# Kernel optimization log

Measured on AMD Instinct MI355X. Metric: run time of the kernel, lower is better.

Reference implementation:

```python
import jax, jax.numpy as jnp
import numpy as np

THRESH = 1.0   # snntorch Leaky default threshold
SLOPE = 25.0   # surrogate.fast_sigmoid(slope=25)
DIM_HEAD = 64
SCALE = DIM_HEAD ** -0.5

# snn.Leaky single step from zero membrane: mem = beta*0 + input = input,
# spike = heaviside(mem - threshold); backward uses fast_sigmoid surrogate.
@jax.custom_vjp
def spike_fn(mem):
    return (mem > THRESH).astype(mem.dtype)

def _spike_fwd(mem):
    return (mem > THRESH).astype(mem.dtype), mem

def _spike_bwd(mem, g):
    return (g / (SLOPE * jnp.abs(mem - THRESH) + 1.0) ** 2,)

spike_fn.defvjp(_spike_fwd, _spike_bwd)

def layer_norm2(x, gamma, beta, eps=1e-5):
    # torch F.layer_norm over x.shape[1:] (last two dims jointly);
    # gamma.repeat(rows,1) == broadcast of gamma over the row axis.
    m = x.mean(axis=(-2, -1), keepdims=True)
    v = x.var(axis=(-2, -1), keepdims=True)
    return (x - m) / jnp.sqrt(v + eps) * gamma + beta

def interp_linear(x, out_len):
    # F.interpolate(mode='linear', align_corners=False) over last axis
    L = x.shape[-1]
    j = jnp.arange(out_len, dtype=x.dtype)
    src = jnp.maximum((j + 0.5) * (L / out_len) - 0.5, 0.0)
    i0 = jnp.clip(jnp.floor(src).astype(jnp.int32), 0, L - 1)
    i1 = jnp.clip(i0 + 1, 0, L - 1)
    w = src - i0.astype(x.dtype)
    return x[..., i0] * (1.0 - w) + x[..., i1] * w

def setup_inputs() -> dict:
    key = jax.random.key(0)
    ks = jax.random.split(key, 8)
    H, N, DIM, HEADS, DH = 4, 512, 8192, 2, 64
    inner = HEADS * DH  # 128; H*inner = 512 (matches fc/conv dims)
    return {
        "pic": jax.random.normal(ks[0], (H, N, DIM), jnp.float32),
        "context": jax.random.normal(ks[1], (H, N, DIM), jnp.float32),
        "gamma": jnp.ones((DIM,), jnp.float32),
        "ln_beta": jnp.zeros((DIM,), jnp.float32),
        "W_pic": jax.random.normal(ks[2], (inner, DIM), jnp.float32) * 0.01,
        "b_pic": jnp.zeros((inner,), jnp.float32),
        "W_ctx": jax.random.normal(ks[3], (2 * DH, DIM), jnp.float32) * 0.01,
        "b_ctx": jnp.zeros((2 * DH,), jnp.float32),
        "conv1_w": jax.random.normal(ks[4], (32, N, 1), jnp.float32) * 0.04,
        "conv1_b": jnp.zeros((32,), jnp.float32),
        "conv2_w": jax.random.normal(ks[5], (1, 32, 1), jnp.float32) * 0.17,
        "conv2_b": jnp.zeros((1,), jnp.float32),
        "fc_w": jax.random.normal(ks[6], (N, N), jnp.float32) * 0.04,
        "fc_b": jnp.zeros((N,), jnp.float32),
    }

def reference(pic, context, gamma, ln_beta, W_pic, b_pic, W_ctx, b_ctx,
              conv1_w, conv1_b, conv2_w, conv2_b, fc_w, fc_b):
    pic = layer_norm2(pic, gamma, ln_beta)          # (H,N,DIM)
    context = layer_norm2(context, gamma, ln_beta)
    # num_steps = batch_size = 1: one SNN step, stack adds leading 'b'=1 axis
    ip_spk = spike_fn(pic)[None]                    # (1,H,N,DIM)
    ic_spk = spike_fn(context)[None]
    ip = (jnp.einsum('bhnd,od->bhno', ip_spk, W_pic) + b_pic) * SCALE  # (1,H,N,128)
    ctx = jnp.einsum('bhnd,od->bhno', ic_spk, W_ctx) + b_ctx           # (1,H,N,128)
    ic, V = jnp.split(ctx, 2, axis=-1)              # (1,H,N,64) each
    # einsum 'b h i d, b h i j -> b h i d': reduce j then broadcast-multiply
    sim = ip * ic.sum(-1, keepdims=True)            # (1,H,N,128)
    attn = jax.nn.softmax(sim, axis=-1)             # (sim - amax then softmax)
    # einsum 'b h i j, b h i d -> b h i j'
    out = attn * V.sum(-1, keepdims=True)           # (1,H,N,128)
    b, h, n, d = out.shape
    out = jnp.transpose(out, (0, 2, 1, 3)).reshape(b, n, h * d)  # (1,512,512)
    ip_sum = ip.sum(axis=3)                         # (1,H,512)
    # resnet: two kernel-size-1 Conv1d == channel-mixing matmuls
    o1 = jnp.einsum('bcl,oc->bol', out, conv1_w[:, :, 0]) + conv1_b[None, :, None]
    o1 = jnp.einsum('bcl,oc->bol', o1, conv2_w[:, :, 0]) + conv2_b[None, :, None]  # (1,1,512)
    o1 = o1 @ fc_w.T + fc_b                         # (1,1,512)
    o1 = o1 + ip_sum                                # broadcast -> (1,H,512)
    o1 = jnp.transpose(o1, (0, 2, 1))               # (1,512,H)
    o1 = interp_linear(o1, 64)                      # (1,512,64)
    ic_sum = ic.sum(axis=1)                         # (1,512,64)
    return jax.nn.relu(jax.nn.relu(o1) + ic_sum)
```

## Files before the change

kernel.cpp:

```cpp
#include <hip/hip_runtime.h>

typedef unsigned short ushort;
typedef unsigned int uint;
typedef __attribute__((ext_vector_type(8))) short short8v;
typedef __attribute__((ext_vector_type(4))) float floatx4;

#define DIMK   8192
#define NPER   512
#define NROWS  2048
#define NCOLS  128
#define KSPLIT 8
#define KCHUNK 1024
#define BK     64
#define NIT    16
#define SLICE_ELEMS 4194304.0

static const size_t STATS_OFF = 0;
static const size_t WB_OFF    = 256;
static const size_t WB_BYTES  = (size_t)2 * 128 * DIMK * 2;
static const size_t P_OFF     = WB_OFF + WB_BYTES;
static const size_t P_BYTES   = (size_t)2 * KSPLIT * NROWS * NCOLS * 4;
static const size_t OUT2_OFF  = P_OFF + P_BYTES;
static const size_t IPSUM_OFF = OUT2_OFF + (size_t)512 * 512 * 4;
static const size_t CTXB_OFF  = IPSUM_OFF + (size_t)4 * 512 * 4;
static const size_t O2_OFF    = CTXB_OFF + (size_t)2048 * 64 * 4;
static const size_t WS_NEED   = O2_OFF + (size_t)512 * 4;

__device__ __forceinline__ ushort f2bf(float x) {
  uint u = __float_as_uint(x);
  return (ushort)((u + 0x7FFFu + ((u >> 16) & 1u)) >> 16);
}

__global__ __launch_bounds__(256) void k_wconv(const float* __restrict__ Wp,
                                               const float* __restrict__ Wc,
                                               ushort* __restrict__ Wb) {
  const size_t i = ((size_t)blockIdx.x * 256 + threadIdx.x) * 8;
  const size_t HALF = (size_t)128 * DIMK;
  const float* src = (i < HALF) ? (Wp + i) : (Wc + (i - HALF));
  float4 a = *(const float4*)src;
  float4 b = *(const float4*)(src + 4);
  short8v v;
  v[0] = (short)f2bf(a.x); v[1] = (short)f2bf(a.y);
  v[2] = (short)f2bf(a.z); v[3] = (short)f2bf(a.w);
  v[4] = (short)f2bf(b.x); v[5] = (short)f2bf(b.y);
  v[6] = (short)f2bf(b.z); v[7] = (short)f2bf(b.w);
  *(short8v*)&Wb[i] = v;
}

__global__ __launch_bounds__(256) void k_stats(const float* __restrict__ pic,
                                               const float* __restrict__ ctx,
                                               double* __restrict__ stats) {
  int b = blockIdx.x;
  int s = b >> 8;
  int c = b & 255;
  int t = s >> 2, h = s & 3;
  const float* base = (t ? ctx : pic) + (size_t)h * NPER * DIMK + (size_t)c * 16384;
  const float4* p4 = reinterpret_cast<const float4*>(base);
  int tid = threadIdx.x;
  float sum = 0.f, sq = 0.f;
#pragma unroll
  for (int i = 0; i < 16; ++i) {
    float4 v = p4[tid + 256 * i];
    sum += (v.x + v.y) + (v.z + v.w);
    sq  += (v.x * v.x + v.y * v.y) + (v.z * v.z + v.w * v.w);
  }
#pragma unroll
  for (int d = 1; d < 64; d <<= 1) {
    sum += __shfl_xor(sum, d);
    sq  += __shfl_xor(sq, d);
  }
  __shared__ float ps[4], pq[4];
  int w = tid >> 6;
  if ((tid & 63) == 0) { ps[w] = sum; pq[w] = sq; }
  __syncthreads();
  if (tid == 0) {
    double S = (double)ps[0] + (double)ps[1] + (double)ps[2] + (double)ps[3];
    double Q = (double)pq[0] + (double)pq[1] + (double)pq[2] + (double)pq[3];
    atomicAdd(&stats[2 * s], S);
    atomicAdd(&stats[2 * s + 1], Q);
  }
}

__global__ __launch_bounds__(256) void k_gemm(const float* __restrict__ pic,
                                              const float* __restrict__ ctxin,
                                              const float* __restrict__ gamma,
                                              const float* __restrict__ lnbeta,
                                              const ushort* __restrict__ Wb,
                                              const double* __restrict__ stats,
                                              float* __restrict__ P) {
  const int tid  = threadIdx.x;
  const int lane = tid & 63;
  const int wv   = tid >> 6;
  const int wm   = wv >> 1, wn = wv & 1;
  const int bx = blockIdx.x, ky = blockIdx.y, t = blockIdx.z;
  const float*  A  = t ? ctxin : pic;
  const ushort* Wt = Wb + (size_t)t * 128 * DIMK;
  const int row0 = bx * 128;

  const int sidx = t * 4 + (bx >> 2);
  double su = stats[2 * sidx], qu = stats[2 * sidx + 1];
  double dmean = su * (1.0 / SLICE_ELEMS);
  const float mean = (float)dmean;
  const float var  = (float)(qu * (1.0 / SLICE_ELEMS) - dmean * dmean);
  const float rstd = rsqrtf(var + 1e-5f);

  __shared__ __align__(16) ushort Asl[2][128 * BK];
  __shared__ __align__(16) ushort Wsl[2][128 * BK];

  const int k8 = tid & 7;
  const int r0 = tid >> 3;

  const int kg8 = (lane >> 4) << 3;
  int abase[4], axor[4], bbase[4], bxor[4];
#pragma unroll
  for (int m = 0; m < 4; ++m) {
    int ra = wm * 64 + m * 16 + (lane & 15);
    abase[m] = ra * BK; axor[m] = (ra & 7) << 3;
    int rb = wn * 64 + m * 16 + (lane & 15);
    bbase[m] = rb * BK; bxor[m] = (rb & 7) << 3;
  }

  floatx4 acc[4][4];
  floatx4 zz = {0.f, 0.f, 0.f, 0.f};
#pragma unroll
  for (int m = 0; m < 4; ++m)
#pragma unroll
    for (int n = 0; n < 4; ++n) acc[m][n] = zz;

  float4 xa[4][2]; uint4 xw[4];
  float4 g0, g1, bb0, bb1;

  auto LOAD = [&](int it) {
    const int kb = ky * KCHUNK + it * BK;
    const float* gp = gamma  + kb + k8 * 8;
    const float* bp = lnbeta + kb + k8 * 8;
    g0 = *(const float4*)gp;  g1 = *(const float4*)(gp + 4);
    bb0 = *(const float4*)bp; bb1 = *(const float4*)(bp + 4);
#pragma unroll
    for (int c = 0; c < 4; ++c) {
      const int r = r0 + c * 32;
      const float* ap = A + (size_t)(row0 + r) * DIMK + kb + k8 * 8;
      xa[c][0] = *(const float4*)ap;
      xa[c][1] = *(const float4*)(ap + 4);
      xw[c] = *(const uint4*)(Wt + (size_t)r * DIMK + kb + k8 * 8);
    }
  };

  auto WRITE = [&](int buf) {
#pragma unroll
    for (int c = 0; c < 4; ++c) {
      const int r = r0 + c * 32;
      float xs[8] = {xa[c][0].x, xa[c][0].y, xa[c][0].z, xa[c][0].w,
                     xa[c][1].x, xa[c][1].y, xa[c][1].z, xa[c][1].w};
      float gs[8] = {g0.x, g0.y, g0.z, g0.w, g1.x, g1.y, g1.z, g1.w};
      float bs[8] = {bb0.x, bb0.y, bb0.z, bb0.w, bb1.x, bb1.y, bb1.z, bb1.w};
      short8v sv;
#pragma unroll
      for (int j = 0; j < 8; ++j)
        sv[j] = (short)(((xs[j] - mean) * rstd * gs[j] + bs[j] > 1.0f) ? 0x3F80 : 0);
      const int off = r * BK + ((k8 * 8) ^ ((r & 7) << 3));
      *(short8v*)&Asl[buf][off] = sv;
      *(uint4*)&Wsl[buf][off]   = xw[c];
    }
  };

  auto COMPUTE = [&](int buf) {
#pragma unroll
    for (int ks = 0; ks < 2; ++ks) {
      short8v af[4], bfr[4];
#pragma unroll
      for (int m = 0; m < 4; ++m)
        af[m] = *(const short8v*)&Asl[buf][abase[m] + ((ks * 32 + kg8) ^ axor[m])];
#pragma unroll
      for (int n = 0; n < 4; ++n)
        bfr[n] = *(const short8v*)&Wsl[buf][bbase[n] + ((ks * 32 + kg8) ^ bxor[n])];
#pragma unroll
      for (int m = 0; m < 4; ++m)
#pragma unroll
        for (int n = 0; n < 4; ++n)
          acc[m][n] = __builtin_amdgcn_mfma_f32_16x16x32_bf16(af[m], bfr[n], acc[m][n], 0, 0, 0);
    }
  };

  LOAD(0);
  WRITE(0);
  __syncthreads();
#pragma unroll 2
  for (int it = 0; it < NIT - 1; ++it) {
    LOAD(it + 1);
    COMPUTE(it & 1);
    __syncthreads();
    WRITE((it + 1) & 1);
    __syncthreads();
  }
  COMPUTE((NIT - 1) & 1);

  float* Pt = P + ((size_t)(t * KSPLIT + ky) * NROWS + row0) * NCOLS;
#pragma unroll
  for (int m = 0; m < 4; ++m) {
    const int gr = wm * 64 + m * 16 + ((lane >> 4) << 2);
#pragma unroll
    for (int n = 0; n < 4; ++n) {
      const int gc = wn * 64 + n * 16 + (lane & 15);
#pragma unroll
      for (int j = 0; j < 4; ++j)
        Pt[(size_t)(gr + j) * NCOLS + gc] = acc[m][n][j];
    }
  }
}

__global__ __launch_bounds__(128) void k_row(const float* __restrict__ P,
                                             const float* __restrict__ b_pic,
                                             const float* __restrict__ b_ctx,
                                             float* __restrict__ out2,
                                             float* __restrict__ ipsum,
                                             float* __restrict__ ctxbuf) {
  const int r = blockIdx.x;
  const int o = threadIdx.x;
  float ipv = b_pic[o];
  float cv  = b_ctx[o];
#pragma unroll
  for (int ks = 0; ks < KSPLIT; ++ks) {
    ipv += P[((size_t)ks * NROWS + r) * NCOLS + o];
    cv  += P[((size_t)(KSPLIT + ks) * NROWS + r) * NCOLS + o];
  }
  ipv *= 0.125f;

  __shared__ float sh[4];
  __shared__ float sh2[2];
  const int w = o >> 6;

  float cs = cv;
  float is = ipv;
#pragma unroll
  for (int d = 1; d < 64; d <<= 1) {
    cs += __shfl_xor(cs, d);
    is += __shfl_xor(is, d);
  }
  if ((o & 63) == 0) { sh[w] = cs; sh[2 + w] = is; }
  __syncthreads();
  const float ic_s = sh[0];
  const float v_s  = sh[1];
  const float ips  = sh[2] + sh[3];
  if (o == 0) ipsum[r] = ips;

  const float sim = ipv * ic_s;
  float m = sim;
#pragma unroll
  for (int d = 1; d < 64; d <<= 1) m = fmaxf(m, __shfl_xor(m, d));
  if ((o & 63) == 0) sh2[w] = m;
  __syncthreads();
  m = fmaxf(sh2[0], sh2[1]);
  const float e = __expf(sim - m);
  float es = e;
#pragma unroll
  for (int d = 1; d < 64; d <<= 1) es += __shfl_xor(es, d);
  if ((o & 63) == 0) sh[w] = es;
  __syncthreads();
  const float denom = sh[0] + sh[1];
  const float outv = (e / denom) * v_s;

  const int hh = r >> 9, n = r & 511;
  out2[(size_t)n * 512 + hh * 128 + o] = outv;
  if (o < 64) ctxbuf[(size_t)r * 64 + o] = cv;
}

__global__ __launch_bounds__(512) void k_mid(const float* __restrict__ out2,
                                             const float* __restrict__ c1w,
                                             const float* __restrict__ c1b,
                                             const float* __restrict__ c2w,
                                             const float* __restrict__ c2b,
                                             float* __restrict__ o2buf) {
  const int b = blockIdx.x;
  const int tid = threadIdx.x;
  __shared__ float wsh[64];
  __shared__ float c2s[32];
  if (tid < 32) c2s[tid] = c2w[tid];
  __syncthreads();
  if (tid < 64) {
    const int n = b * 64 + tid;
    float a = 0.f;
#pragma unroll
    for (int o = 0; o < 32; ++o) a += c2s[o] * c1w[o * 512 + n];
    wsh[tid] = a;
  }
  __syncthreads();
  float acc = 0.f;
#pragma unroll 8
  for (int u = 0; u < 64; ++u)
    acc += out2[(size_t)(b * 64 + u) * 512 + tid] * wsh[u];
  if (b == 0) {
    float beff = c2b[0];
#pragma unroll
    for (int o = 0; o < 32; ++o) beff += c2s[o] * c1b[o];
    acc += beff;
  }
  atomicAdd(&o2buf[tid], acc);
}

__global__ __launch_bounds__(64) void k_final(const float* __restrict__ o2buf,
                                              const float* __restrict__ fcw,
                                              const float* __restrict__ fcb,
                                              const float* __restrict__ ipsum,
                                              const float* __restrict__ ctxbuf,
                                              float* __restrict__ out) {
  const int i = blockIdx.x;
  const int j = threadIdx.x;
  float a = 0.f;
#pragma unroll
  for (int u = 0; u < 8; ++u) {
    const int k = j * 8 + u;
    a += o2buf[k] * fcw[(size_t)i * 512 + k];
  }
#pragma unroll
  for (int d = 1; d < 64; d <<= 1) a += __shfl_xor(a, d);
  const float o3 = a + fcb[i];

  float src = (j + 0.5f) * (4.0f / 64.0f) - 0.5f;
  src = fmaxf(src, 0.0f);
  int i0 = (int)floorf(src);
  if (i0 > 3) i0 = 3;
  const int i1 = (i0 + 1 < 3) ? i0 + 1 : 3;
  const float w = src - (float)i0;

  const float v0 = o3 + ipsum[i0 * 512 + i];
  const float v1 = o3 + ipsum[i1 * 512 + i];
  float v = v0 * (1.0f - w) + v1 * w;
  v = fmaxf(v, 0.0f);

  float ics = 0.f;
#pragma unroll
  for (int hh2 = 0; hh2 < 4; ++hh2) ics += ctxbuf[((size_t)hh2 * 512 + i) * 64 + j];
  out[(size_t)i * 64 + j] = fmaxf(v + ics, 0.0f);
}

extern "C" void kernel_launch(void* const* d_in, const int* in_sizes, int n_in,
                              void* d_out, int out_size, void* d_ws, size_t ws_size,
                              hipStream_t stream) {
  const float* pic    = (const float*)d_in[0];
  const float* ctx    = (const float*)d_in[1];
  const float* gamma  = (const float*)d_in[2];
  const float* lnbeta = (const float*)d_in[3];
  const float* Wp     = (const float*)d_in[4];
  const float* bp     = (const float*)d_in[5];
  const float* Wc     = (const float*)d_in[6];
  const float* bc     = (const float*)d_in[7];
  const float* c1w    = (const float*)d_in[8];
  const float* c1b    = (const float*)d_in[9];
  const float* c2w    = (const float*)d_in[10];
  const float* c2b    = (const float*)d_in[11];
  const float* fcw    = (const float*)d_in[12];
  const float* fcb    = (const float*)d_in[13];
  float* out = (float*)d_out;

  if (ws_size < WS_NEED) return;

  char* ws = (char*)d_ws;
  double* stats = (double*)(ws + STATS_OFF);
  ushort* Wb    = (ushort*)(ws + WB_OFF);
  float* P      = (float*)(ws + P_OFF);
  float* out2   = (float*)(ws + OUT2_OFF);
  float* ipsum  = (float*)(ws + IPSUM_OFF);
  float* ctxbuf = (float*)(ws + CTXB_OFF);
  float* o2buf  = (float*)(ws + O2_OFF);

  hipMemsetAsync(stats, 0, 256, stream);
  hipMemsetAsync(o2buf, 0, 512 * 4, stream);
  k_wconv<<<1024, 256, 0, stream>>>(Wp, Wc, Wb);
  k_stats<<<2048, 256, 0, stream>>>(pic, ctx, stats);
  k_gemm<<<dim3(16, KSPLIT, 2), 256, 0, stream>>>(pic, ctx, gamma, lnbeta, Wb, stats, P);
  k_row<<<NROWS, 128, 0, stream>>>(P, bp, bc, out2, ipsum, ctxbuf);
  k_mid<<<8, 512, 0, stream>>>(out2, c1w, c1b, c2w, c2b, o2buf);
  k_final<<<512, 64, 0, stream>>>(o2buf, fcw, fcb, ipsum, ctxbuf, out);
}
```

Before: 245.8 us.

## Fuse weight conversion into stats, halve GEMM tile rows, vectorize row kernel

Merges the bf16 weight conversion into the stats kernel as extra blocks and combines the two memsets into one, which removes a launch and an async op. The stats blocks now cover half as much data each, so there are more blocks. The GEMM M-tile shrinks from 128 to 64 rows with launch bounds set for 2 blocks, doubling the grid to 512 blocks to improve CU occupancy at the cost of reloading weight tiles twice as often. The row kernel processes 8 rows per block with float4 loads and wave-level reductions instead of block-wide syncs.

```diff
diff --git a/kernel.cpp b/kernel.cpp
--- a/kernel.cpp
+++ b/kernel.cpp
@@ -12,65 +12,73 @@
 #define KSPLIT 8
 #define KCHUNK 1024
 #define BK     64
+#define BM     64
 #define NIT    16
 #define SLICE_ELEMS 4194304.0
 
 static const size_t STATS_OFF = 0;
-static const size_t WB_OFF    = 256;
+static const size_t O2_OFF    = 128;
+static const size_t WB_OFF    = 4096;
 static const size_t WB_BYTES  = (size_t)2 * 128 * DIMK * 2;
 static const size_t P_OFF     = WB_OFF + WB_BYTES;
 static const size_t P_BYTES   = (size_t)2 * KSPLIT * NROWS * NCOLS * 4;
 static const size_t OUT2_OFF  = P_OFF + P_BYTES;
 static const size_t IPSUM_OFF = OUT2_OFF + (size_t)512 * 512 * 4;
 static const size_t CTXB_OFF  = IPSUM_OFF + (size_t)4 * 512 * 4;
-static const size_t O2_OFF    = CTXB_OFF + (size_t)2048 * 64 * 4;
-static const size_t WS_NEED   = O2_OFF + (size_t)512 * 4;
+static const size_t WS_NEED   = CTXB_OFF + (size_t)2048 * 64 * 4;
 
 __device__ __forceinline__ ushort f2bf(float x) {
   uint u = __float_as_uint(x);
   return (ushort)((u + 0x7FFFu + ((u >> 16) & 1u)) >> 16);
 }
 
-__global__ __launch_bounds__(256) void k_wconv(const float* __restrict__ Wp,
-                                               const float* __restrict__ Wc,
-                                               ushort* __restrict__ Wb) {
-  const size_t i = ((size_t)blockIdx.x * 256 + threadIdx.x) * 8;
-  const size_t HALF = (size_t)128 * DIMK;
-  const float* src = (i < HALF) ? (Wp + i) : (Wc + (i - HALF));
-  float4 a = *(const float4*)src;
-  float4 b = *(const float4*)(src + 4);
-  short8v v;
-  v[0] = (short)f2bf(a.x); v[1] = (short)f2bf(a.y);
-  v[2] = (short)f2bf(a.z); v[3] = (short)f2bf(a.w);
-  v[4] = (short)f2bf(b.x); v[5] = (short)f2bf(b.y);
-  v[6] = (short)f2bf(b.z); v[7] = (short)f2bf(b.w);
-  *(short8v*)&Wb[i] = v;
-}
-
 __global__ __launch_bounds__(256) void k_stats(const float* __restrict__ pic,
                                                const float* __restrict__ ctx,
-                                               double* __restrict__ stats) {
-  int b = blockIdx.x;
-  int s = b >> 8;
-  int c = b & 255;
-  int t = s >> 2, h = s & 3;
-  const float* base = (t ? ctx : pic) + (size_t)h * NPER * DIMK + (size_t)c * 16384;
-  const float4* p4 = reinterpret_cast<const float4*>(base);
-  int tid = threadIdx.x;
-  float sum = 0.f, sq = 0.f;
-#pragma unroll
-  for (int i = 0; i < 16; ++i) {
-    float4 v = p4[tid + 256 * i];
-    sum += (v.x + v.y) + (v.z + v.w);
-    sq  += (v.x * v.x + v.y * v.y) + (v.z * v.z + v.w * v.w);
-  }
+                                               const float* __restrict__ Wp,
+                                               const float* __restrict__ Wc,
+                                               double* __restrict__ stats,
+                                               ushort* __restrict__ Wb) {
+  const int bid = blockIdx.x;
+  const int tid = threadIdx.x;
+  if (bid >= 4096) {
+    const size_t i = ((size_t)(bid - 4096) * 256 + tid) * 8;
+    const size_t HALF = (size_t)128 * DIMK;
+    const float* src = (i < HALF) ? (Wp + i) : (Wc + (i - HALF));
+    float4 a = *(const float4*)src;
+    float4 b = *(const float4*)(src + 4);
+    short8v v;
+    v[0] = (short)f2bf(a.x); v[1] = (short)f2bf(a.y);
+    v[2] = (short)f2bf(a.z); v[3] = (short)f2bf(a.w);
+    v[4] = (short)f2bf(b.x); v[5] = (short)f2bf(b.y);
+    v[6] = (short)f2bf(b.z); v[7] = (short)f2bf(b.w);
+    *(short8v*)&Wb[i] = v;
+    return;
+  }
+  const int s = bid >> 9;
+  const int c = bid & 511;
+  const int t = s >> 2, h = s & 3;
+  const float4* p4 = reinterpret_cast<const float4*>(
+      (t ? ctx : pic) + (size_t)h * NPER * DIMK + (size_t)c * 8192);
+  float4 v[8];
+#pragma unroll
+  for (int j = 0; j < 8; ++j) v[j] = p4[tid + 256 * j];
+  float s0 = 0.f, s1 = 0.f, q0 = 0.f, q1 = 0.f;
+#pragma unroll
+  for (int j = 0; j < 8; j += 2) {
+    s0 += (v[j].x + v[j].y) + (v[j].z + v[j].w);
+    q0 += (v[j].x * v[j].x + v[j].y * v[j].y) + (v[j].z * v[j].z + v[j].w * v[j].w);
+    s1 += (v[j + 1].x + v[j + 1].y) + (v[j + 1].z + v[j + 1].w);
+    q1 += (v[j + 1].x * v[j + 1].x + v[j + 1].y * v[j + 1].y) +
+          (v[j + 1].z * v[j + 1].z + v[j + 1].w * v[j + 1].w);
+  }
+  float sum = s0 + s1, sq = q0 + q1;
 #pragma unroll
   for (int d = 1; d < 64; d <<= 1) {
     sum += __shfl_xor(sum, d);
     sq  += __shfl_xor(sq, d);
   }
   __shared__ float ps[4], pq[4];
-  int w = tid >> 6;
+  const int w = tid >> 6;
   if ((tid & 63) == 0) { ps[w] = sum; pq[w] = sq; }
   __syncthreads();
   if (tid == 0) {
@@ -81,13 +89,13 @@
   }
 }
 
-__global__ __launch_bounds__(256) void k_gemm(const float* __restrict__ pic,
-                                              const float* __restrict__ ctxin,
-                                              const float* __restrict__ gamma,
-                                              const float* __restrict__ lnbeta,
-                                              const ushort* __restrict__ Wb,
-                                              const double* __restrict__ stats,
-                                              float* __restrict__ P) {
+__global__ __launch_bounds__(256, 2) void k_gemm(const float* __restrict__ pic,
+                                                 const float* __restrict__ ctxin,
+                                                 const float* __restrict__ gamma,
+                                                 const float* __restrict__ lnbeta,
+                                                 const ushort* __restrict__ Wb,
+                                                 const double* __restrict__ stats,
+                                                 float* __restrict__ P) {
   const int tid  = threadIdx.x;
   const int lane = tid & 63;
   const int wv   = tid >> 6;
@@ -95,60 +103,64 @@
   const int bx = blockIdx.x, ky = blockIdx.y, t = blockIdx.z;
   const float*  A  = t ? ctxin : pic;
   const ushort* Wt = Wb + (size_t)t * 128 * DIMK;
-  const int row0 = bx * 128;
-
-  const int sidx = t * 4 + (bx >> 2);
+  const int row0 = bx * BM;
+
+  const int sidx = t * 4 + (bx >> 3);
   double su = stats[2 * sidx], qu = stats[2 * sidx + 1];
   double dmean = su * (1.0 / SLICE_ELEMS);
   const float mean = (float)dmean;
   const float var  = (float)(qu * (1.0 / SLICE_ELEMS) - dmean * dmean);
   const float rstd = rsqrtf(var + 1e-5f);
 
-  __shared__ __align__(16) ushort Asl[2][128 * BK];
+  __shared__ __align__(16) ushort Asl[2][BM * BK];
   __shared__ __align__(16) ushort Wsl[2][128 * BK];
 
-  const int k8 = tid & 7;
+  const int k8 = (tid & 7) * 8;
   const int r0 = tid >> 3;
 
   const int kg8 = (lane >> 4) << 3;
-  int abase[4], axor[4], bbase[4], bxor[4];
-#pragma unroll
-  for (int m = 0; m < 4; ++m) {
-    int ra = wm * 64 + m * 16 + (lane & 15);
+  int abase[2], axor[2], bbase[4], bxor[4];
+#pragma unroll
+  for (int m = 0; m < 2; ++m) {
+    const int ra = wm * 32 + m * 16 + (lane & 15);
     abase[m] = ra * BK; axor[m] = (ra & 7) << 3;
-    int rb = wn * 64 + m * 16 + (lane & 15);
-    bbase[m] = rb * BK; bxor[m] = (rb & 7) << 3;
-  }
-
-  floatx4 acc[4][4];
+  }
+#pragma unroll
+  for (int n = 0; n < 4; ++n) {
+    const int rb = wn * 64 + n * 16 + (lane & 15);
+    bbase[n] = rb * BK; bxor[n] = (rb & 7) << 3;
+  }
+
+  floatx4 acc[2][4];
   floatx4 zz = {0.f, 0.f, 0.f, 0.f};
 #pragma unroll
-  for (int m = 0; m < 4; ++m)
+  for (int m = 0; m < 2; ++m)
 #pragma unroll
     for (int n = 0; n < 4; ++n) acc[m][n] = zz;
 
-  float4 xa[4][2]; uint4 xw[4];
+  float4 xa[2][2]; uint4 xw[4];
   float4 g0, g1, bb0, bb1;
 
   auto LOAD = [&](int it) {
     const int kb = ky * KCHUNK + it * BK;
-    const float* gp = gamma  + kb + k8 * 8;
-    const float* bp = lnbeta + kb + k8 * 8;
+    const float* gp = gamma  + kb + k8;
+    const float* bp = lnbeta + kb + k8;
     g0 = *(const float4*)gp;  g1 = *(const float4*)(gp + 4);
     bb0 = *(const float4*)bp; bb1 = *(const float4*)(bp + 4);
 #pragma unroll
-    for (int c = 0; c < 4; ++c) {
-      const int r = r0 + c * 32;
-      const float* ap = A + (size_t)(row0 + r) * DIMK + kb + k8 * 8;
+    for (int c = 0; c < 2; ++c) {
+      const float* ap = A + (size_t)(row0 + r0 + c * 32) * DIMK + kb + k8;
       xa[c][0] = *(const float4*)ap;
       xa[c][1] = *(const float4*)(ap + 4);
-      xw[c] = *(const uint4*)(Wt + (size_t)r * DIMK + kb + k8 * 8);
-    }
+    }
+#pragma unroll
+    for (int c = 0; c < 4; ++c)
+      xw[c] = *(const uint4*)(Wt + (size_t)(r0 + c * 32) * DIMK + kb + k8);
   };
 
   auto WRITE = [&](int buf) {
 #pragma unroll
-    for (int c = 0; c < 4; ++c) {
+    for (int c = 0; c < 2; ++c) {
       const int r = r0 + c * 32;
       float xs[8] = {xa[c][0].x, xa[c][0].y, xa[c][0].z, xa[c][0].w,
                      xa[c][1].x, xa[c][1].y, xa[c][1].z, xa[c][1].w};
@@ -158,24 +170,27 @@
 #pragma unroll
       for (int j = 0; j < 8; ++j)
         sv[j] = (short)(((xs[j] - mean) * rstd * gs[j] + bs[j] > 1.0f) ? 0x3F80 : 0);
-      const int off = r * BK + ((k8 * 8) ^ ((r & 7) << 3));
-      *(short8v*)&Asl[buf][off] = sv;
-      *(uint4*)&Wsl[buf][off]   = xw[c];
+      *(short8v*)&Asl[buf][r * BK + (k8 ^ ((r & 7) << 3))] = sv;
+    }
+#pragma unroll
+    for (int c = 0; c < 4; ++c) {
+      const int r = r0 + c * 32;
+      *(uint4*)&Wsl[buf][r * BK + (k8 ^ ((r & 7) << 3))] = xw[c];
     }
   };
 
   auto COMPUTE = [&](int buf) {
 #pragma unroll
     for (int ks = 0; ks < 2; ++ks) {
-      short8v af[4], bfr[4];
-#pragma unroll
-      for (int m = 0; m < 4; ++m)
+      short8v af[2], bfr[4];
+#pragma unroll
+      for (int m = 0; m < 2; ++m)
         af[m] = *(const short8v*)&Asl[buf][abase[m] + ((ks * 32 + kg8) ^ axor[m])];
 #pragma unroll
       for (int n = 0; n < 4; ++n)
         bfr[n] = *(const short8v*)&Wsl[buf][bbase[n] + ((ks * 32 + kg8) ^ bxor[n])];
 #pragma unroll
-      for (int m = 0; m < 4; ++m)
+      for (int m = 0; m < 2; ++m)
 #pragma unroll
         for (int n = 0; n < 4; ++n)
           acc[m][n] = __builtin_amdgcn_mfma_f32_16x16x32_bf16(af[m], bfr[n], acc[m][n], 0, 0, 0);
@@ -197,8 +212,8 @@
 
   float* Pt = P + ((size_t)(t * KSPLIT + ky) * NROWS + row0) * NCOLS;
 #pragma unroll
-  for (int m = 0; m < 4; ++m) {
-    const int gr = wm * 64 + m * 16 + ((lane >> 4) << 2);
+  for (int m = 0; m < 2; ++m) {
+    const int gr = wm * 32 + m * 16 + ((lane >> 4) << 2);
 #pragma unroll
     for (int n = 0; n < 4; ++n) {
       const int gc = wn * 64 + n * 16 + (lane & 15);
@@ -209,60 +224,59 @@
   }
 }
 
-__global__ __launch_bounds__(128) void k_row(const float* __restrict__ P,
+__global__ __launch_bounds__(256) void k_row(const float* __restrict__ P,
                                              const float* __restrict__ b_pic,
                                              const float* __restrict__ b_ctx,
                                              float* __restrict__ out2,
                                              float* __restrict__ ipsum,
                                              float* __restrict__ ctxbuf) {
-  const int r = blockIdx.x;
-  const int o = threadIdx.x;
-  float ipv = b_pic[o];
-  float cv  = b_ctx[o];
+  const int tid = threadIdx.x;
+  const int q = tid >> 5;
+  const int u = tid & 31;
+  const int r = blockIdx.x * 8 + q;
+  const int o4 = u * 4;
+
+  float4 ip = ((const float4*)b_pic)[u];
+  float4 cv = ((const float4*)b_ctx)[u];
 #pragma unroll
   for (int ks = 0; ks < KSPLIT; ++ks) {
-    ipv += P[((size_t)ks * NROWS + r) * NCOLS + o];
-    cv  += P[((size_t)(KSPLIT + ks) * NROWS + r) * NCOLS + o];
-  }
-  ipv *= 0.125f;
-
-  __shared__ float sh[4];
-  __shared__ float sh2[2];
-  const int w = o >> 6;
-
-  float cs = cv;
-  float is = ipv;
-#pragma unroll
-  for (int d = 1; d < 64; d <<= 1) {
-    cs += __shfl_xor(cs, d);
-    is += __shfl_xor(is, d);
-  }
-  if ((o & 63) == 0) { sh[w] = cs; sh[2 + w] = is; }
-  __syncthreads();
-  const float ic_s = sh[0];
-  const float v_s  = sh[1];
-  const float ips  = sh[2] + sh[3];
-  if (o == 0) ipsum[r] = ips;
-
-  const float sim = ipv * ic_s;
-  float m = sim;
-#pragma unroll
-  for (int d = 1; d < 64; d <<= 1) m = fmaxf(m, __shfl_xor(m, d));
-  if ((o & 63) == 0) sh2[w] = m;
-  __syncthreads();
-  m = fmaxf(sh2[0], sh2[1]);
-  const float e = __expf(sim - m);
-  float es = e;
-#pragma unroll
-  for (int d = 1; d < 64; d <<= 1) es += __shfl_xor(es, d);
-  if ((o & 63) == 0) sh[w] = es;
-  __syncthreads();
-  const float denom = sh[0] + sh[1];
-  const float outv = (e / denom) * v_s;
+    const float4 a = *(const float4*)&P[((size_t)ks * NROWS + r) * NCOLS + o4];
+    const float4 b = *(const float4*)&P[((size_t)(KSPLIT + ks) * NROWS + r) * NCOLS + o4];
+    ip.x += a.x; ip.y += a.y; ip.z += a.z; ip.w += a.w;
+    cv.x += b.x; cv.y += b.y; cv.z += b.z; cv.w += b.w;
+  }
+  ip.x *= 0.125f; ip.y *= 0.125f; ip.z *= 0.125f; ip.w *= 0.125f;
+
+  float clo = (u < 16) ? (cv.x + cv.y) + (cv.z + cv.w) : 0.f;
+  float chi = (u >= 16) ? (cv.x + cv.y) + (cv.z + cv.w) : 0.f;
+  float ipp = (ip.x + ip.y) + (ip.z + ip.w);
+#pragma unroll
+  for (int d = 1; d < 32; d <<= 1) {
+    clo += __shfl_xor(clo, d);
+    chi += __shfl_xor(chi, d);
+    ipp += __shfl_xor(ipp, d);
+  }
+  const float ic_s = clo, v_s = chi;
+  if (u == 0) ipsum[r] = ipp;
+
+  float4 sim;
+  sim.x = ip.x * ic_s; sim.y = ip.y * ic_s; sim.z = ip.z * ic_s; sim.w = ip.w * ic_s;
+  float m = fmaxf(fmaxf(sim.x, sim.y), fmaxf(sim.z, sim.w));
+#pragma unroll
+  for (int d = 1; d < 32; d <<= 1) m = fmaxf(m, __shfl_xor(m, d));
+  float4 e;
+  e.x = __expf(sim.x - m); e.y = __expf(sim.y - m);
+  e.z = __expf(sim.z - m); e.w = __expf(sim.w - m);
+  float es = (e.x + e.y) + (e.z + e.w);
+#pragma unroll
+  for (int d = 1; d < 32; d <<= 1) es += __shfl_xor(es, d);
+  const float sc = v_s / es;
+  float4 outv;
+  outv.x = e.x * sc; outv.y = e.y * sc; outv.z = e.z * sc; outv.w = e.w * sc;
 
   const int hh = r >> 9, n = r & 511;
-  out2[(size_t)n * 512 + hh * 128 + o] = outv;
-  if (o < 64) ctxbuf[(size_t)r * 64 + o] = cv;
+  *(float4*)&out2[(size_t)n * 512 + hh * 128 + o4] = outv;
+  if (u < 16) *(float4*)&ctxbuf[(size_t)r * 64 + o4] = cv;
 }
 
 __global__ __launch_bounds__(512) void k_mid(const float* __restrict__ out2,
@@ -287,8 +301,8 @@
   __syncthreads();
   float acc = 0.f;
 #pragma unroll 8
-  for (int u = 0; u < 64; ++u)
-    acc += out2[(size_t)(b * 64 + u) * 512 + tid] * wsh[u];
+  for (int ucnt = 0; ucnt < 64; ++ucnt)
+    acc += out2[(size_t)(b * 64 + ucnt) * 512 + tid] * wsh[ucnt];
   if (b == 0) {
     float beff = c2b[0];
 #pragma unroll
@@ -308,8 +322,8 @@
   const int j = threadIdx.x;
   float a = 0.f;
 #pragma unroll
-  for (int u = 0; u < 8; ++u) {
-    const int k = j * 8 + u;
+  for (int uu = 0; uu < 8; ++uu) {
+    const int k = j * 8 + uu;
     a += o2buf[k] * fcw[(size_t)i * 512 + k];
   }
 #pragma unroll
@@ -357,19 +371,17 @@
 
   char* ws = (char*)d_ws;
   double* stats = (double*)(ws + STATS_OFF);
+  float* o2buf  = (float*)(ws + O2_OFF);
   ushort* Wb    = (ushort*)(ws + WB_OFF);
   float* P      = (float*)(ws + P_OFF);
   float* out2   = (float*)(ws + OUT2_OFF);
   float* ipsum  = (float*)(ws + IPSUM_OFF);
   float* ctxbuf = (float*)(ws + CTXB_OFF);
-  float* o2buf  = (float*)(ws + O2_OFF);
-
-  hipMemsetAsync(stats, 0, 256, stream);
-  hipMemsetAsync(o2buf, 0, 512 * 4, stream);
-  k_wconv<<<1024, 256, 0, stream>>>(Wp, Wc, Wb);
-  k_stats<<<2048, 256, 0, stream>>>(pic, ctx, stats);
-  k_gemm<<<dim3(16, KSPLIT, 2), 256, 0, stream>>>(pic, ctx, gamma, lnbeta, Wb, stats, P);
-  k_row<<<NROWS, 128, 0, stream>>>(P, bp, bc, out2, ipsum, ctxbuf);
+
+  hipMemsetAsync(ws, 0, 128 + 512 * 4, stream);
+  k_stats<<<5120, 256, 0, stream>>>(pic, ctx, Wp, Wc, stats, Wb);
+  k_gemm<<<dim3(32, KSPLIT, 2), 256, 0, stream>>>(pic, ctx, gamma, lnbeta, Wb, stats, P);
+  k_row<<<256, 256, 0, stream>>>(P, bp, bc, out2, ipsum, ctxbuf);
   k_mid<<<8, 512, 0, stream>>>(out2, c1w, c1b, c2w, c2b, o2buf);
   k_final<<<512, 64, 0, stream>>>(o2buf, fcw, fcb, ipsum, ctxbuf, out);
 }
```

New measurement: 283.2 us. +15.2%, slower.
